# Optimization experiments

Measured on AMD Instinct MI355X. Metric: run time of the kernel, lower is better.

The kernel has to match this reference:

```python
import jax, jax.numpy as jnp
import numpy as np

PS = 8  # window_size
LOCAL = 16  # split channels

def conv1x1(x, w, b):
    return jnp.einsum('oi,bihw->bohw', w, x) + b[None, :, None, None]

def dynamic_local(x, w1, b1, w2, b2, k):
    # x: (B, C, H, W); dynamic per-(batch,channel) depthwise conv with generated kernels
    B, C, H, W = x.shape
    pooled = x.mean((2, 3))                      # (B, C) adaptive avg pool to 1x1
    h = jax.nn.relu(pooled @ w1.T + b1)
    kern = (h @ w2.T + b2).reshape(B, C, k, k)   # per-sample depthwise kernels
    def per_batch(xb, kb):
        return jax.lax.conv_general_dilated(
            xb[None], kb[:, None], (1, 1), 'SAME',
            feature_group_count=C,
            dimension_numbers=('NCHW', 'OIHW', 'NCHW'))[0]
    return jax.vmap(per_batch)(x, kern)

def channel_layernorm(x, w, b, eps=1e-6):
    # LayerNorm over channel dim (torch module's non-channels_last path)
    u = x.mean(1, keepdims=True)
    s = ((x - u) ** 2).mean(1, keepdims=True)
    xn = (x - u) / jnp.sqrt(s + eps)
    return w[None, :, None, None] * xn + b[None, :, None, None]

def fsas(x, hid_w, hid_b, dw_w, dw_b, ln_w, ln_b, out_w, out_b):
    hidden = conv1x1(x, hid_w, hid_b)
    mid = hidden.shape[1]
    dw = jax.lax.conv_general_dilated(
        hidden, dw_w[:, None], (1, 1), 'SAME',
        feature_group_count=mid,
        dimension_numbers=('NCHW', 'OIHW', 'NCHW')) + dw_b[None, :, None, None]
    q, k, v = jnp.split(dw, 3, axis=1)
    B, C, H, W = q.shape
    def patch(t):
        # (B,C,H,W) -> (B,C,H/ps,W/ps,ps,ps)
        return t.reshape(B, C, H // PS, PS, W // PS, PS).transpose(0, 1, 2, 4, 3, 5)
    qf = jnp.fft.rfft2(patch(q))
    kf = jnp.fft.rfft2(patch(k))
    out = jnp.fft.irfft2(qf * kf, s=(PS, PS))
    out = out.transpose(0, 1, 2, 4, 3, 5).reshape(B, C, H, W)
    out = channel_layernorm(out, ln_w, ln_b)
    return conv1x1(v * out, out_w, out_b)


def setup_inputs() -> dict:
    key = jax.random.key(0)
    ks = jax.random.split(key, 12)
    s = 0.02
    return {
        'x': jax.random.normal(ks[0], (4, 64, 256, 256), jnp.float32),
        'dl1_w1': jax.random.normal(ks[1], (16, 16), jnp.float32) * s,
        'dl1_b1': jnp.zeros((16,), jnp.float32),
        'dl1_w2': jax.random.normal(ks[2], (144, 16), jnp.float32) * s,
        'dl1_b2': jnp.zeros((144,), jnp.float32),
        'dl2_w1': jax.random.normal(ks[3], (16, 16), jnp.float32) * s,
        'dl2_b1': jnp.zeros((16,), jnp.float32),
        'dl2_w2': jax.random.normal(ks[4], (400, 16), jnp.float32) * s,
        'dl2_b2': jnp.zeros((400,), jnp.float32),
        'fs_hid_w': jax.random.normal(ks[5], (144, 48), jnp.float32) * s,
        'fs_hid_b': jnp.zeros((144,), jnp.float32),
        'fs_dw_w': jax.random.normal(ks[6], (144, 3, 3), jnp.float32) * s,
        'fs_dw_b': jnp.zeros((144,), jnp.float32),
        'fs_ln_w': jnp.ones((48,), jnp.float32),
        'fs_ln_b': jnp.zeros((48,), jnp.float32),
        'fs_out_w': jax.random.normal(ks[7], (48, 48), jnp.float32) * s,
        'fs_out_b': jnp.zeros((48,), jnp.float32),
        'last_w': jax.random.normal(ks[8], (64, 64), jnp.float32) * s,
        'last_b': jnp.zeros((64,), jnp.float32),
    }


def reference(x, dl1_w1, dl1_b1, dl1_w2, dl1_b2, dl2_w1, dl2_b1, dl2_w2, dl2_b2,
              fs_hid_w, fs_hid_b, fs_dw_w, fs_dw_b, fs_ln_w, fs_ln_b,
              fs_out_w, fs_out_b, last_w, last_b):
    x1, x2 = x[:, :LOCAL], x[:, LOCAL:]
    x1 = dynamic_local(x1, dl1_w1, dl1_b1, dl1_w2, dl1_b2, 3)
    x1 = dynamic_local(x1, dl2_w1, dl2_b1, dl2_w2, dl2_b2, 5)
    x2 = fsas(x2, fs_hid_w, fs_hid_b, fs_dw_w, fs_dw_b, fs_ln_w, fs_ln_b, fs_out_w, fs_out_b)
    return conv1x1(jnp.concatenate([x1, x2], axis=1), last_w, last_b)
```

## Files before the change

### kernel.cpp

```cpp
#include <hip/hip_runtime.h>

typedef _Float16 h2 __attribute__((ext_vector_type(2)));
typedef _Float16 h4 __attribute__((ext_vector_type(4)));
typedef _Float16 h8 __attribute__((ext_vector_type(8)));
typedef float f4 __attribute__((ext_vector_type(4)));

#if defined(__has_builtin)
#if __has_builtin(__builtin_amdgcn_fdot2)
#define HAS_FDOT2 1
#endif
#endif

__device__ __forceinline__ float warpsum(float v) {
    for (int off = 32; off > 0; off >>= 1) v += __shfl_down(v, off);
    return v;
}

__global__ __launch_bounds__(256) void k_prep(const float* __restrict__ hid_w,
                                              const float* __restrict__ out_w,
                                              const float* __restrict__ last_w,
                                              _Float16* __restrict__ hwH,
                                              _Float16* __restrict__ owlwH) {
    int t = blockIdx.x * 256 + threadIdx.x;
    int stride = gridDim.x * 256;
    for (int i = t; i < 10368; i += stride) {
        int n = i / 72, k = i - n * 72;
        hwH[i] = (k < 48) ? (_Float16)hid_w[n * 48 + k] : (_Float16)0.f;
    }
    for (int i = t; i < 3456; i += stride) {
        int n = i / 72, k = i - n * 72;
        owlwH[i] = (k < 48) ? (_Float16)out_w[n * 48 + k] : (_Float16)0.f;
    }
    for (int i = t; i < 4608; i += stride) {
        int n = i / 72, k = i - n * 72;
        owlwH[3456 + i] = (k < 64) ? (_Float16)last_w[n * 64 + k] : (_Float16)0.f;
    }
}

__global__ __launch_bounds__(256) void k_pool(const float* __restrict__ x, float* __restrict__ pooled1) {
    int bid = blockIdx.x;
    int b = bid >> 4, c = bid & 15;
    const float* base = x + (size_t)(b * 64 + c) * 65536;
    float s = 0.f;
    for (int i = threadIdx.x; i < 16384; i += 256) {
        float4 v = ((const float4*)base)[i];
        s += v.x + v.y + v.z + v.w;
    }
    __shared__ float red[4];
    s = warpsum(s);
    if ((threadIdx.x & 63) == 0) red[threadIdx.x >> 6] = s;
    __syncthreads();
    if (threadIdx.x == 0) pooled1[bid] = (red[0] + red[1] + red[2] + red[3]) * (1.f / 65536.f);
}

__global__ __launch_bounds__(256) void k_kern1(const float* __restrict__ pooled1,
                                               const float* __restrict__ w1, const float* __restrict__ b1,
                                               const float* __restrict__ w2, const float* __restrict__ b2,
                                               float* __restrict__ kern1) {
    __shared__ float h[64];
    int t = threadIdx.x;
    if (t < 64) {
        int b = t >> 4, j = t & 15;
        float a = b1[j];
        for (int i = 0; i < 16; ++i) a += pooled1[b * 16 + i] * w1[j * 16 + i];
        h[t] = fmaxf(a, 0.f);
    }
    __syncthreads();
    for (int i = t; i < 576; i += 256) {
        int b = i / 144, o = i - b * 144;
        float a = b2[o];
        for (int j = 0; j < 16; ++j) a += h[b * 16 + j] * w2[o * 16 + j];
        kern1[i] = a;
    }
}

__global__ __launch_bounds__(256) void k_dw3(const float* __restrict__ x,
                                             const float* __restrict__ kern1,
                                             float* __restrict__ y1, float* __restrict__ rowsum) {
    __shared__ float tile[10][258];
    __shared__ float red[8][4];
    int bid = blockIdx.x;
    int rb = bid & 31, bc = bid >> 5;
    int b = bc >> 4, c = bc & 15;
    int row0 = rb << 3;
    int col = threadIdx.x;
    const float* xc = x + ((size_t)(b * 64 + c) << 16);
#pragma unroll
    for (int j = 0; j < 10; ++j) {
        int r = row0 - 1 + j;
        tile[j][col + 1] = ((unsigned)r < 256u) ? xc[(r << 8) + col] : 0.f;
    }
    if (col < 10) { tile[col][0] = 0.f; tile[col][257] = 0.f; }
    const float* k9 = kern1 + b * 144 + c * 9;
    float kk[9];
#pragma unroll
    for (int i = 0; i < 9; ++i) kk[i] = k9[i];
    __syncthreads();
#pragma unroll
    for (int j = 0; j < 8; ++j) {
        float acc = 0.f;
#pragma unroll
        for (int dy = 0; dy < 3; ++dy)
#pragma unroll
            for (int dx = 0; dx < 3; ++dx)
                acc += kk[dy * 3 + dx] * tile[j + dy][col + dx];
        y1[((size_t)bc << 16) + ((row0 + j) << 8) + col] = acc;
        float s = warpsum(acc);
        if ((col & 63) == 0) red[j][col >> 6] = s;
    }
    __syncthreads();
    if (col < 8) rowsum[bc * 256 + row0 + col] = red[col][0] + red[col][1] + red[col][2] + red[col][3];
}

__global__ __launch_bounds__(256) void k_kern2(const float* __restrict__ rowsum,
                                               const float* __restrict__ w1, const float* __restrict__ b1,
                                               const float* __restrict__ w2, const float* __restrict__ b2,
                                               float* __restrict__ kern2) {
    __shared__ float ps[256];
    __shared__ float p2[64];
    __shared__ float h[64];
    int t = threadIdx.x;
    {
        int pair = t >> 2, seg = t & 3;
        const float* rs = rowsum + pair * 256 + seg * 64;
        float s = 0.f;
        for (int j = 0; j < 64; ++j) s += rs[j];
        ps[t] = s;
    }
    __syncthreads();
    if (t < 64) p2[t] = (ps[t * 4] + ps[t * 4 + 1] + ps[t * 4 + 2] + ps[t * 4 + 3]) * (1.f / 65536.f);
    __syncthreads();
    if (t < 64) {
        int b = t >> 4, j = t & 15;
        float a = b1[j];
        for (int i = 0; i < 16; ++i) a += p2[b * 16 + i] * w1[j * 16 + i];
        h[t] = fmaxf(a, 0.f);
    }
    __syncthreads();
    for (int i = t; i < 1600; i += 256) {
        int b = i / 400, o = i - b * 400;
        float a = b2[o];
        for (int j = 0; j < 16; ++j) a += h[b * 16 + j] * w2[o * 16 + j];
        kern2[i] = a;
    }
}

__global__ __launch_bounds__(256) void k_dw5(const float* __restrict__ y1,
                                             const float* __restrict__ kern2,
                                             float* __restrict__ x1o) {
    __shared__ float tile[12][260];
    int bid = blockIdx.x;
    int rb = bid & 31, bc = bid >> 5;
    int b = bc >> 4, c = bc & 15;
    int row0 = rb << 3;
    int col = threadIdx.x;
    const float* yc = y1 + ((size_t)bc << 16);
#pragma unroll
    for (int j = 0; j < 12; ++j) {
        int r = row0 - 2 + j;
        tile[j][col + 2] = ((unsigned)r < 256u) ? yc[(r << 8) + col] : 0.f;
    }
    if (col < 12) { tile[col][0] = 0.f; tile[col][1] = 0.f; tile[col][258] = 0.f; tile[col][259] = 0.f; }
    const float* k25 = kern2 + b * 400 + c * 25;
    float kk[25];
#pragma unroll
    for (int i = 0; i < 25; ++i) kk[i] = k25[i];
    __syncthreads();
#pragma unroll
    for (int j = 0; j < 8; ++j) {
        float acc = 0.f;
#pragma unroll
        for (int dy = 0; dy < 5; ++dy)
#pragma unroll
            for (int dx = 0; dx < 5; ++dx)
                acc += kk[dy * 5 + dx] * tile[j + dy][col + dx];
        x1o[((size_t)bc << 16) + ((row0 + j) << 8) + col] = acc;
    }
}

__global__ __launch_bounds__(512, 6) void k_fsas(const float* __restrict__ x,
                                                 const _Float16* __restrict__ hwH, const float* __restrict__ hid_b,
                                                 const float* __restrict__ dw_w, const float* __restrict__ dw_b,
                                                 const float* __restrict__ ln_w, const float* __restrict__ ln_b,
                                                 const _Float16* __restrict__ owlwH, const float* __restrict__ out_b,
                                                 const float* __restrict__ last_b,
                                                 const float* __restrict__ x1o, float* __restrict__ out) {
    __shared__ __align__(16) _Float16 Abuf[10368];
    __shared__ __align__(16) _Float16 hbuf[5760];
    __shared__ __align__(16) _Float16 qbuf[3456];
    __shared__ __align__(16) _Float16 kbuf2[6528];
    __shared__ __align__(16) float pstat[128];

    _Float16* fbuf  = Abuf;
    float*    lnp   = (float*)(Abuf + 4608);
    _Float16* vbuf  = Abuf + 6656;
    _Float16* outb  = hbuf;
    _Float16* cbuf  = hbuf;
    _Float16* sbufA = kbuf2;

    int tid = threadIdx.x;
    int lane = tid & 63;
    int wave = __builtin_amdgcn_readfirstlane(tid >> 6);
    int bid = blockIdx.x;
    int swz = ((bid & 7) << 9) | (bid >> 3);
    int b = swz >> 10;
    int rem = swz & 1023;
    int row0 = (rem >> 5) << 3, col0 = (rem & 31) << 3;

    int px2 = lane, pr = wave;
    size_t gpix2 = ((size_t)(row0 + (px2 >> 3)) << 8) + col0 + (px2 & 7);

    int l16 = lane & 15, lhi = lane >> 4;
    int fr = l16 * 72 + (lhi << 3);
    int mb = wave * 16 + (lhi << 2);
    bool st[4], vok[4];
#pragma unroll
    for (int r = 0; r < 4; ++r) {
        int m = mb + r;
        st[r] = (m < 120);
        int yv = m / 12, xv = m - yv * 12;
        vok[r] = st[r] && (xv < 10) &&
                 ((unsigned)(row0 - 1 + yv) < 256u) && ((unsigned)(col0 - 1 + xv) < 256u);
    }

    for (int j = tid; j < 4608; j += 512) ((unsigned int*)Abuf)[j] = 0u;
    __syncthreads();

    for (int j = tid; j < 4800; j += 512) {
        int k = j / 100, q = j - k * 100;
        int yv = q / 10, xv = q - yv * 10;
        int gy = row0 - 1 + yv, gx = col0 - 1 + xv;
        if ((unsigned)gy < 256u && (unsigned)gx < 256u)
            Abuf[(yv * 12 + xv) * 72 + k] = (_Float16)x[((size_t)(b * 64 + 16 + k) << 16) + (gy << 8) + gx];
    }
    __syncthreads();

    h8 a0 = *(const h8*)(Abuf + wave * 1152 + fr);
    h8 a1 = *(const h8*)(Abuf + wave * 1152 + 32 + fr);

    int dch = tid >> 3, drow = tid & 7;

#pragma unroll 1
    for (int ph = 0; ph < 3; ++ph) {
        const _Float16* wp = hwH + ph * 3456;
        h8 b0[3], b1[3];
#pragma unroll
        for (int nt = 0; nt < 3; ++nt) {
            b0[nt] = *(const h8*)(wp + nt * 1152 + fr);
            b1[nt] = *(const h8*)(wp + nt * 1152 + 32 + fr);
        }
#pragma unroll
        for (int nt = 0; nt < 3; ++nt) {
            float bias = hid_b[ph * 48 + nt * 16 + l16];
            f4 acc = {bias, bias, bias, bias};
            acc = __builtin_amdgcn_mfma_f32_16x16x32_f16(a0, b0[nt], acc, 0, 0, 0);
            acc = __builtin_amdgcn_mfma_f32_16x16x32_f16(a1, b1[nt], acc, 0, 0, 0);
            int n_l = nt * 16 + l16;
#pragma unroll
            for (int r = 0; r < 4; ++r)
                if (st[r]) hbuf[n_l * 120 + mb + r] = vok[r] ? (_Float16)acc[r] : (_Float16)0.f;
        }
        __syncthreads();
        if (tid < 384) {
            int c = ph * 48 + dch;
            const float* dwp = dw_w + c * 9;
            float bias = dw_b[c];
            float o[8];
#pragma unroll
            for (int xx = 0; xx < 8; ++xx) o[xx] = bias;
            const _Float16* hb = hbuf + dch * 120 + drow * 12;
#pragma unroll
            for (int dy = 0; dy < 3; ++dy) {
                h4 r0 = *(const h4*)(hb + dy * 12);
                h4 r1 = *(const h4*)(hb + dy * 12 + 4);
                h2 r2 = *(const h2*)(hb + dy * 12 + 8);
                float rowv[10] = {(float)r0[0], (float)r0[1], (float)r0[2], (float)r0[3],
                                  (float)r1[0], (float)r1[1], (float)r1[2], (float)r1[3],
                                  (float)r2[0], (float)r2[1]};
                float w0 = dwp[dy * 3], w1 = dwp[dy * 3 + 1], w2 = dwp[dy * 3 + 2];
#pragma unroll
                for (int xx = 0; xx < 8; ++xx)
                    o[xx] += w0 * rowv[xx] + w1 * rowv[xx + 1] + w2 * rowv[xx + 2];
            }
            if (ph == 0) {
                h8 qv;
#pragma unroll
                for (int xx = 0; xx < 8; ++xx) qv[xx] = (_Float16)o[xx];
                *(h8*)(qbuf + dch * 72 + drow * 8) = qv;
            } else if (ph == 1) {
                h8 kr, ko;
#pragma unroll
                for (int t2 = 0; t2 < 8; ++t2) {
                    kr[t2] = (_Float16)o[(8 - t2) & 7];
                    ko[t2] = (_Float16)o[(9 - t2) & 7];
                }
                *(h8*)(kbuf2 + dch * 136 + drow * 16) = kr;
                *(h8*)(kbuf2 + dch * 136 + drow * 16 + 8) = ko;
            } else {
                h8 vv;
#pragma unroll
                for (int xx = 0; xx < 8; ++xx) vv[xx] = (_Float16)o[xx];
                *(h8*)(vbuf + dch * 72 + drow * 8) = vv;
            }
        }
        __syncthreads();
    }

    float xa = x1o[((size_t)(b * 16 + 2 * pr) << 16) + gpix2];
    float xb = x1o[((size_t)(b * 16 + 2 * pr + 1) << 16) + gpix2];

    if (tid < 384) {
        int ch = tid >> 3, m = tid & 7;
        float co[8];
#pragma unroll
        for (int n = 0; n < 8; ++n) co[n] = 0.f;
#pragma unroll
        for (int i8 = 0; i8 < 8; ++i8) {
            int r = (m - i8) & 7;
            h8 q8 = *(const h8*)(qbuf + ch * 72 + i8 * 8);
            h8 e8 = *(const h8*)(kbuf2 + ch * 136 + r * 16);
#ifdef HAS_FDOT2
            h8 o8 = *(const h8*)(kbuf2 + ch * 136 + r * 16 + 8);
            h2 qp[4], ep[4], op[4];
            qp[0] = __builtin_shufflevector(q8, q8, 0, 1); qp[1] = __builtin_shufflevector(q8, q8, 2, 3);
            qp[2] = __builtin_shufflevector(q8, q8, 4, 5); qp[3] = __builtin_shufflevector(q8, q8, 6, 7);
            ep[0] = __builtin_shufflevector(e8, e8, 0, 1); ep[1] = __builtin_shufflevector(e8, e8, 2, 3);
            ep[2] = __builtin_shufflevector(e8, e8, 4, 5); ep[3] = __builtin_shufflevector(e8, e8, 6, 7);
            op[0] = __builtin_shufflevector(o8, o8, 0, 1); op[1] = __builtin_shufflevector(o8, o8, 2, 3);
            op[2] = __builtin_shufflevector(o8, o8, 4, 5); op[3] = __builtin_shufflevector(o8, o8, 6, 7);
#pragma unroll
            for (int u = 0; u < 4; ++u)
#pragma unroll
                for (int a = 0; a < 4; ++a) {
                    co[2 * u]     = __builtin_amdgcn_fdot2(qp[a], ep[(a - u) & 3], co[2 * u], false);
                    co[2 * u + 1] = __builtin_amdgcn_fdot2(qp[a], op[(a - u) & 3], co[2 * u + 1], false);
                }
#else
            float qf[8], kf[8];
#pragma unroll
            for (int j = 0; j < 8; ++j) { qf[j] = (float)q8[j]; kf[j] = (float)e8[(8 - j) & 7]; }
#pragma unroll
            for (int j = 0; j < 8; ++j)
#pragma unroll
                for (int n = 0; n < 8; ++n)
                    co[n] += qf[j] * kf[(n - j) & 7];
#endif
        }
#pragma unroll
        for (int v = 0; v < 4; ++v)
            *(h2*)(outb + ch * 72 + m * 8 + 2 * v) = (h2){(_Float16)co[2 * v], (_Float16)co[2 * v + 1]};
    }
    *(h2*)(fbuf + px2 * 72 + 2 * pr) = (h2){(_Float16)xa, (_Float16)xb};
    __syncthreads();

    {
        float s = 0.f, ss = 0.f;
#pragma unroll
        for (int cc = 0; cc < 6; ++cc) {
            float v = (float)outb[(pr * 6 + cc) * 72 + px2];
            s += v; ss += v * v;
        }
        lnp[pr * 64 + px2] = s;
        lnp[512 + pr * 64 + px2] = ss;
    }
    __syncthreads();
    if (tid < 64) {
        float s = 0.f, ss = 0.f;
#pragma unroll
        for (int g = 0; g < 8; ++g) { s += lnp[g * 64 + tid]; ss += lnp[512 + g * 64 + tid]; }
        float mu = s * (1.f / 48.f);
        float var = ss * (1.f / 48.f) - mu * mu;
        pstat[tid * 2] = mu;
        pstat[tid * 2 + 1] = rsqrtf(var + 1e-6f);
    }
    __syncthreads();

    {
        float mu = pstat[lane * 2], inv = pstat[lane * 2 + 1];
        int cl0 = wave * 6;
#pragma unroll
        for (int u = 0; u < 6; ++u) {
            int cl = cl0 + u;
            float o = (float)outb[cl * 72 + lane];
            float vv = (float)vbuf[cl * 72 + lane];
            float lnv = ln_w[cl] * ((o - mu) * inv) + ln_b[cl];
            sbufA[lane * 72 + cl] = (_Float16)(vv * lnv);
        }
        *(h2*)(sbufA + px2 * 72 + 48 + 2 * pr) = (h2){(_Float16)0.f, (_Float16)0.f};
    }
    __syncthreads();

    for (int t = wave; t < 12; t += 8) {
        int mt = t / 3, nt = t - mt * 3;
        h8 c0 = *(const h8*)(sbufA + mt * 1152 + fr);
        h8 c1 = *(const h8*)(sbufA + mt * 1152 + 32 + fr);
        h8 d0 = *(const h8*)(owlwH + nt * 1152 + fr);
        h8 d1 = *(const h8*)(owlwH + nt * 1152 + 32 + fr);
        float bias = out_b[nt * 16 + l16];
        f4 acc = {bias, bias, bias, bias};
        acc = __builtin_amdgcn_mfma_f32_16x16x32_f16(c0, d0, acc, 0, 0, 0);
        acc = __builtin_amdgcn_mfma_f32_16x16x32_f16(c1, d1, acc, 0, 0, 0);
        int n5 = nt * 16 + l16;
        int pb = mt * 16 + (lhi << 2);
#pragma unroll
        for (int r = 0; r < 4; ++r)
            fbuf[(pb + r) * 72 + 16 + n5] = (_Float16)acc[r];
    }
    __syncthreads();

    for (int t = wave; t < 16; t += 8) {
        int mt = t >> 2, nt = t & 3;
        h8 c0 = *(const h8*)(fbuf + mt * 1152 + fr);
        h8 c1 = *(const h8*)(fbuf + mt * 1152 + 32 + fr);
        h8 d0 = *(const h8*)(owlwH + 3456 + nt * 1152 + fr);
        h8 d1 = *(const h8*)(owlwH + 3456 + nt * 1152 + 32 + fr);
        float bias = last_b[nt * 16 + l16];
        f4 acc = {bias, bias, bias, bias};
        acc = __builtin_amdgcn_mfma_f32_16x16x32_f16(c0, d0, acc, 0, 0, 0);
        acc = __builtin_amdgcn_mfma_f32_16x16x32_f16(c1, d1, acc, 0, 0, 0);
        int ch = nt * 16 + l16;
        int pb = mt * 16 + (lhi << 2);
#pragma unroll
        for (int r = 0; r < 4; ++r)
            cbuf[ch * 72 + pb + r] = (_Float16)acc[r];
    }
    __syncthreads();

#pragma unroll
    for (int u = 0; u < 8; ++u) {
        int ch = pr * 8 + u;
        out[((size_t)(b * 64 + ch) << 16) + gpix2] = (float)cbuf[ch * 72 + px2];
    }
}

extern "C" void kernel_launch(void* const* d_in, const int* in_sizes, int n_in,
                              void* d_out, int out_size, void* d_ws, size_t ws_size,
                              hipStream_t stream) {
    const float* x      = (const float*)d_in[0];
    const float* dl1_w1 = (const float*)d_in[1];
    const float* dl1_b1 = (const float*)d_in[2];
    const float* dl1_w2 = (const float*)d_in[3];
    const float* dl1_b2 = (const float*)d_in[4];
    const float* dl2_w1 = (const float*)d_in[5];
    const float* dl2_b1 = (const float*)d_in[6];
    const float* dl2_w2 = (const float*)d_in[7];
    const float* dl2_b2 = (const float*)d_in[8];
    const float* hid_w  = (const float*)d_in[9];
    const float* hid_b  = (const float*)d_in[10];
    const float* dw_w   = (const float*)d_in[11];
    const float* dw_b   = (const float*)d_in[12];
    const float* ln_w   = (const float*)d_in[13];
    const float* ln_b   = (const float*)d_in[14];
    const float* out_w  = (const float*)d_in[15];
    const float* out_b  = (const float*)d_in[16];
    const float* last_w = (const float*)d_in[17];
    const float* last_b = (const float*)d_in[18];
    float* out = (float*)d_out;

    float* ws      = (float*)d_ws;
    float* pooled1 = ws;
    float* kern1   = ws + 64;
    float* rowsum  = ws + 1024;
    float* kern2   = ws + 17408;
    _Float16* hwH   = (_Float16*)(ws + 19008);
    _Float16* owlwH = (_Float16*)(ws + 24192);
    float* y1      = ws + 32768;
    float* x1o     = ws + 32768 + 4194304;

    k_prep <<<8,    256, 0, stream>>>(hid_w, out_w, last_w, hwH, owlwH);
    k_pool <<<64,   256, 0, stream>>>(x, pooled1);
    k_kern1<<<1,    256, 0, stream>>>(pooled1, dl1_w1, dl1_b1, dl1_w2, dl1_b2, kern1);
    k_dw3  <<<2048, 256, 0, stream>>>(x, kern1, y1, rowsum);
    k_kern2<<<1,    256, 0, stream>>>(rowsum, dl2_w1, dl2_b1, dl2_w2, dl2_b2, kern2);
    k_dw5  <<<2048, 256, 0, stream>>>(y1, kern2, x1o);
    k_fsas <<<4096, 512, 0, stream>>>(x, hwH, hid_b, dw_w, dw_b, ln_w, ln_b,
                                      owlwH, out_b, last_b, x1o, out);
}
```

Before: 179.8 us.

## Shrink fsas LDS footprint with swizzled layouts and register-held v for higher occupancy

Cuts the k_fsas shared-memory footprint by aliasing hbuf into Abuf, keeping v and the circular-conv outputs in registers, and tightening the q and output strides. Raises the launch-bounds occupancy target from 6 to 8 waves. Adds XOR-swizzled LDS layouts for the MFMA operand buffers to reduce bank conflicts. Writes the final conv output straight from MFMA accumulators as float4 global stores, dropping the cbuf staging pass. The register pressure from holding v and co, plus the occupancy target, may cause spills.

New measurement: 176.8 us. About the same (-1.6%).

```diff
diff --git a/kernel.cpp b/kernel.cpp
--- a/kernel.cpp
+++ b/kernel.cpp
@@ -14,6 +14,13 @@
 __device__ __forceinline__ float warpsum(float v) {
     for (int off = 32; off > 0; off >>= 1) v += __shfl_down(v, off);
     return v;
+}
+
+__device__ __forceinline__ int aswz(int p, int k) {
+    return p * 72 + ((((k >> 3) ^ (p >> 3)) & 7) << 3) + (k & 7);
+}
+__device__ __forceinline__ int sswz(int p, int k) {
+    return p * 64 + ((((k >> 3) ^ (p >> 3)) & 7) << 3) + (k & 7);
 }
 
 __global__ __launch_bounds__(256) void k_prep(const float* __restrict__ hid_w,
@@ -178,24 +185,22 @@
     }
 }
 
-__global__ __launch_bounds__(512, 6) void k_fsas(const float* __restrict__ x,
+__global__ __launch_bounds__(512, 8) void k_fsas(const float* __restrict__ x,
                                                  const _Float16* __restrict__ hwH, const float* __restrict__ hid_b,
                                                  const float* __restrict__ dw_w, const float* __restrict__ dw_b,
                                                  const float* __restrict__ ln_w, const float* __restrict__ ln_b,
                                                  const _Float16* __restrict__ owlwH, const float* __restrict__ out_b,
                                                  const float* __restrict__ last_b,
                                                  const float* __restrict__ x1o, float* __restrict__ out) {
-    __shared__ __align__(16) _Float16 Abuf[10368];
-    __shared__ __align__(16) _Float16 hbuf[5760];
-    __shared__ __align__(16) _Float16 qbuf[3456];
+    __shared__ __align__(16) _Float16 Abuf[9824];
+    __shared__ __align__(16) _Float16 qbuf[3072];
     __shared__ __align__(16) _Float16 kbuf2[6528];
     __shared__ __align__(16) float pstat[128];
 
+    _Float16* hbuf  = Abuf;
     _Float16* fbuf  = Abuf;
     float*    lnp   = (float*)(Abuf + 4608);
-    _Float16* vbuf  = Abuf + 6656;
-    _Float16* outb  = hbuf;
-    _Float16* cbuf  = hbuf;
+    _Float16* outb  = Abuf + 6656;
     _Float16* sbufA = kbuf2;
 
     int tid = threadIdx.x;
@@ -207,11 +212,7 @@
     int rem = swz & 1023;
     int row0 = (rem >> 5) << 3, col0 = (rem & 31) << 3;
 
-    int px2 = lane, pr = wave;
-    size_t gpix2 = ((size_t)(row0 + (px2 >> 3)) << 8) + col0 + (px2 & 7);
-
     int l16 = lane & 15, lhi = lane >> 4;
-    int fr = l16 * 72 + (lhi << 3);
     int mb = wave * 16 + (lhi << 2);
     bool st[4], vok[4];
 #pragma unroll
@@ -223,38 +224,49 @@
                  ((unsigned)(row0 - 1 + yv) < 256u) && ((unsigned)(col0 - 1 + xv) < 256u);
     }
 
-    for (int j = tid; j < 4608; j += 512) ((unsigned int*)Abuf)[j] = 0u;
-    __syncthreads();
-
-    for (int j = tid; j < 4800; j += 512) {
-        int k = j / 100, q = j - k * 100;
-        int yv = q / 10, xv = q - yv * 10;
+    for (int j = tid; j < 5760; j += 512) {
+        int k = j / 120, p = j - k * 120;
+        int yv = p / 12, xv = p - yv * 12;
         int gy = row0 - 1 + yv, gx = col0 - 1 + xv;
-        if ((unsigned)gy < 256u && (unsigned)gx < 256u)
-            Abuf[(yv * 12 + xv) * 72 + k] = (_Float16)x[((size_t)(b * 64 + 16 + k) << 16) + (gy << 8) + gx];
-    }
-    __syncthreads();
-
-    h8 a0 = *(const h8*)(Abuf + wave * 1152 + fr);
-    h8 a1 = *(const h8*)(Abuf + wave * 1152 + 32 + fr);
+        float v = 0.f;
+        if (xv < 10 && (unsigned)gy < 256u && (unsigned)gx < 256u)
+            v = x[((size_t)(b * 64 + 16 + k) << 16) + (gy << 8) + gx];
+        Abuf[aswz(p, k)] = (_Float16)v;
+    }
+    for (int j = tid; j < 2048; j += 512) {
+        int p = j >> 4, k = 48 + (j & 15);
+        Abuf[aswz(p, k)] = (_Float16)0.f;
+    }
+    if (tid < 384) {
+        int p = 120 + (tid / 48), k = tid % 48;
+        Abuf[aswz(p, k)] = (_Float16)0.f;
+    }
+    __syncthreads();
+
+    int arow = wave * 16 + l16;
+    h8 a0 = *(const h8*)(Abuf + aswz(arow, lhi << 3));
+    h8 a1 = *(const h8*)(Abuf + aswz(arow, 32 + (lhi << 3)));
+    __syncthreads();
+
+    int px2 = lane, pr = wave;
+    size_t gpix2 = ((size_t)(row0 + (px2 >> 3)) << 8) + col0 + (px2 & 7);
+    float xa = x1o[((size_t)(b * 16 + 2 * pr) << 16) + gpix2];
+    float xb = x1o[((size_t)(b * 16 + 2 * pr + 1) << 16) + gpix2];
 
     int dch = tid >> 3, drow = tid & 7;
+    h8 vreg;
 
 #pragma unroll 1
     for (int ph = 0; ph < 3; ++ph) {
         const _Float16* wp = hwH + ph * 3456;
-        h8 b0[3], b1[3];
-#pragma unroll
+#pragma unroll 1
         for (int nt = 0; nt < 3; ++nt) {
-            b0[nt] = *(const h8*)(wp + nt * 1152 + fr);
-            b1[nt] = *(const h8*)(wp + nt * 1152 + 32 + fr);
-        }
-#pragma unroll
-        for (int nt = 0; nt < 3; ++nt) {
+            h8 b0 = *(const h8*)(wp + nt * 1152 + l16 * 72 + (lhi << 3));
+            h8 b1 = *(const h8*)(wp + nt * 1152 + l16 * 72 + 32 + (lhi << 3));
             float bias = hid_b[ph * 48 + nt * 16 + l16];
             f4 acc = {bias, bias, bias, bias};
-            acc = __builtin_amdgcn_mfma_f32_16x16x32_f16(a0, b0[nt], acc, 0, 0, 0);
-            acc = __builtin_amdgcn_mfma_f32_16x16x32_f16(a1, b1[nt], acc, 0, 0, 0);
+            acc = __builtin_amdgcn_mfma_f32_16x16x32_f16(a0, b0, acc, 0, 0, 0);
+            acc = __builtin_amdgcn_mfma_f32_16x16x32_f16(a1, b1, acc, 0, 0, 0);
             int n_l = nt * 16 + l16;
 #pragma unroll
             for (int r = 0; r < 4; ++r)
@@ -286,7 +298,7 @@
                 h8 qv;
 #pragma unroll
                 for (int xx = 0; xx < 8; ++xx) qv[xx] = (_Float16)o[xx];
-                *(h8*)(qbuf + dch * 72 + drow * 8) = qv;
+                *(h8*)(qbuf + dch * 64 + drow * 8) = qv;
             } else if (ph == 1) {
                 h8 kr, ko;
 #pragma unroll
@@ -297,27 +309,24 @@
                 *(h8*)(kbuf2 + dch * 136 + drow * 16) = kr;
                 *(h8*)(kbuf2 + dch * 136 + drow * 16 + 8) = ko;
             } else {
-                h8 vv;
-#pragma unroll
-                for (int xx = 0; xx < 8; ++xx) vv[xx] = (_Float16)o[xx];
-                *(h8*)(vbuf + dch * 72 + drow * 8) = vv;
+#pragma unroll
+                for (int xx = 0; xx < 8; ++xx) vreg[xx] = (_Float16)o[xx];
             }
         }
         __syncthreads();
     }
 
-    float xa = x1o[((size_t)(b * 16 + 2 * pr) << 16) + gpix2];
-    float xb = x1o[((size_t)(b * 16 + 2 * pr + 1) << 16) + gpix2];
-
+    *(h2*)(fbuf + aswz(px2, 2 * pr)) = (h2){(_Float16)xa, (_Float16)xb};
+
+    float co[8];
     if (tid < 384) {
-        int ch = tid >> 3, m = tid & 7;
-        float co[8];
+        int ch = dch, m = drow;
 #pragma unroll
         for (int n = 0; n < 8; ++n) co[n] = 0.f;
 #pragma unroll
         for (int i8 = 0; i8 < 8; ++i8) {
             int r = (m - i8) & 7;
-            h8 q8 = *(const h8*)(qbuf + ch * 72 + i8 * 8);
+            h8 q8 = *(const h8*)(qbuf + ch * 64 + i8 * 8);
             h8 e8 = *(const h8*)(kbuf2 + ch * 136 + r * 16);
 #ifdef HAS_FDOT2
             h8 o8 = *(const h8*)(kbuf2 + ch * 136 + r * 16 + 8);
@@ -348,20 +357,20 @@
         }
 #pragma unroll
         for (int v = 0; v < 4; ++v)
-            *(h2*)(outb + ch * 72 + m * 8 + 2 * v) = (h2){(_Float16)co[2 * v], (_Float16)co[2 * v + 1]};
-    }
-    *(h2*)(fbuf + px2 * 72 + 2 * pr) = (h2){(_Float16)xa, (_Float16)xb};
+            *(h2*)(outb + dch * 66 + drow * 8 + 2 * v) = (h2){(_Float16)co[2 * v], (_Float16)co[2 * v + 1]};
+    }
     __syncthreads();
 
     {
+        int px = tid & 63, g = tid >> 6;
         float s = 0.f, ss = 0.f;
 #pragma unroll
         for (int cc = 0; cc < 6; ++cc) {
-            float v = (float)outb[(pr * 6 + cc) * 72 + px2];
+            float v = (float)outb[(g * 6 + cc) * 66 + px];
             s += v; ss += v * v;
         }
-        lnp[pr * 64 + px2] = s;
-        lnp[512 + pr * 64 + px2] = ss;
+        lnp[g * 64 + px] = s;
+        lnp[512 + g * 64 + px] = ss;
     }
     __syncthreads();
     if (tid < 64) {
@@ -375,27 +384,27 @@
     }
     __syncthreads();
 
-    {
-        float mu = pstat[lane * 2], inv = pstat[lane * 2 + 1];
-        int cl0 = wave * 6;
-#pragma unroll
-        for (int u = 0; u < 6; ++u) {
-            int cl = cl0 + u;
-            float o = (float)outb[cl * 72 + lane];
-            float vv = (float)vbuf[cl * 72 + lane];
-            float lnv = ln_w[cl] * ((o - mu) * inv) + ln_b[cl];
-            sbufA[lane * 72 + cl] = (_Float16)(vv * lnv);
+    if (tid < 384) {
+        int ch = dch, m = drow;
+        float lw = ln_w[ch], lb = ln_b[ch];
+        const float* ps = pstat + m * 16;
+#pragma unroll
+        for (int n = 0; n < 8; ++n) {
+            float mu = ps[2 * n], inv = ps[2 * n + 1];
+            float lnv = lw * ((co[n] - mu) * inv) + lb;
+            sbufA[sswz(m * 8 + n, ch)] = (_Float16)((float)vreg[n] * lnv);
         }
-        *(h2*)(sbufA + px2 * 72 + 48 + 2 * pr) = (h2){(_Float16)0.f, (_Float16)0.f};
-    }
+    }
+    *(h2*)(sbufA + sswz(px2, 48 + ((tid >> 6) << 1))) = (h2){(_Float16)0.f, (_Float16)0.f};
     __syncthreads();
 
     for (int t = wave; t < 12; t += 8) {
         int mt = t / 3, nt = t - mt * 3;
-        h8 c0 = *(const h8*)(sbufA + mt * 1152 + fr);
-        h8 c1 = *(const h8*)(sbufA + mt * 1152 + 32 + fr);
-        h8 d0 = *(const h8*)(owlwH + nt * 1152 + fr);
-        h8 d1 = *(const h8*)(owlwH + nt * 1152 + 32 + fr);
+        int row5 = mt * 16 + l16;
+        h8 c0 = *(const h8*)(sbufA + sswz(row5, lhi << 3));
+        h8 c1 = *(const h8*)(sbufA + sswz(row5, 32 + (lhi << 3)));
+        h8 d0 = *(const h8*)(owlwH + nt * 1152 + l16 * 72 + (lhi << 3));
+        h8 d1 = *(const h8*)(owlwH + nt * 1152 + l16 * 72 + 32 + (lhi << 3));
         float bias = out_b[nt * 16 + l16];
         f4 acc = {bias, bias, bias, bias};
         acc = __builtin_amdgcn_mfma_f32_16x16x32_f16(c0, d0, acc, 0, 0, 0);
@@ -404,32 +413,25 @@
         int pb = mt * 16 + (lhi << 2);
 #pragma unroll
         for (int r = 0; r < 4; ++r)
-            fbuf[(pb + r) * 72 + 16 + n5] = (_Float16)acc[r];
+            fbuf[aswz(pb + r, 16 + n5)] = (_Float16)acc[r];
     }
     __syncthreads();
 
     for (int t = wave; t < 16; t += 8) {
         int mt = t >> 2, nt = t & 3;
-        h8 c0 = *(const h8*)(fbuf + mt * 1152 + fr);
-        h8 c1 = *(const h8*)(fbuf + mt * 1152 + 32 + fr);
-        h8 d0 = *(const h8*)(owlwH + 3456 + nt * 1152 + fr);
-        h8 d1 = *(const h8*)(owlwH + 3456 + nt * 1152 + 32 + fr);
+        int row6 = mt * 16 + l16;
+        h8 c0 = *(const h8*)(fbuf + aswz(row6, lhi << 3));
+        h8 c1 = *(const h8*)(fbuf + aswz(row6, 32 + (lhi << 3)));
+        h8 d0 = *(const h8*)(owlwH + 3456 + nt * 1152 + l16 * 72 + (lhi << 3));
+        h8 d1 = *(const h8*)(owlwH + 3456 + nt * 1152 + l16 * 72 + 32 + (lhi << 3));
         float bias = last_b[nt * 16 + l16];
         f4 acc = {bias, bias, bias, bias};
         acc = __builtin_amdgcn_mfma_f32_16x16x32_f16(c0, d0, acc, 0, 0, 0);
         acc = __builtin_amdgcn_mfma_f32_16x16x32_f16(c1, d1, acc, 0, 0, 0);
         int ch = nt * 16 + l16;
-        int pb = mt * 16 + (lhi << 2);
-#pragma unroll
-        for (int r = 0; r < 4; ++r)
-            cbuf[ch * 72 + pb + r] = (_Float16)acc[r];
-    }
-    __syncthreads();
-
-#pragma unroll
-    for (int u = 0; u < 8; ++u) {
-        int ch = pr * 8 + u;
-        out[((size_t)(b * 64 + ch) << 16) + gpix2] = (float)cbuf[ch * 72 + px2];
+        int px0 = mt * 16 + (lhi << 2);
+        float4 val = {acc[0], acc[1], acc[2], acc[3]};
+        *(float4*)(out + ((size_t)(b * 64 + ch) << 16) + ((size_t)(row0 + (px0 >> 3)) << 8) + col0 + (px0 & 7)) = val;
     }
 }
 
```
